# Performance work log

Hardware: AMD Instinct MI355X
Metric: run time of the kernel (lower is better)

The kernel has to match this reference:

```python
import jax, jax.numpy as jnp
import numpy as np

B, S, D, H = 2, 2048, 1024, 16
HD = D // H  # 64
EPS = 1e-8


def setup_inputs() -> dict:
    key = jax.random.key(0)
    ks = jax.random.split(key, 9)
    hidden_states = jax.random.normal(ks[0], (B, S, D), dtype=jnp.float32)
    # rotary tables: standard RoPE angles over half the head dim
    pos = jnp.arange(S, dtype=jnp.float32)[:, None]
    inv_freq = 1.0 / (10000.0 ** (jnp.arange(0, HD, 2, dtype=jnp.float32) / HD))  # [HD/2]
    ang = pos * inv_freq[None, :]  # [S, HD/2]
    sin = jnp.sin(ang)[None, None]  # [1,1,S,HD/2]
    cos = jnp.cos(ang)[None, None]
    s = 1.0 / np.sqrt(D)
    wq = jax.random.normal(ks[1], (D, D), dtype=jnp.float32) * s
    wk = jax.random.normal(ks[2], (D, D), dtype=jnp.float32) * s
    wv = jax.random.normal(ks[3], (D, D), dtype=jnp.float32) * s
    wo = jax.random.normal(ks[4], (D, D), dtype=jnp.float32) * s
    bo = jnp.zeros((D,), dtype=jnp.float32)
    scale = jnp.ones((D,), dtype=jnp.float32)
    return {"hidden_states": hidden_states, "sin": sin, "cos": cos,
            "wq": wq, "wk": wk, "wv": wv, "wo": wo, "bo": bo, "scale": scale}


def _heads(x):
    # [B,S,D] -> [B,H,S,HD]
    return x.reshape(B, S, H, HD).transpose(0, 2, 1, 3)


def _rotary(x, sin, cos):
    # interleaved RoPE: even/odd pairs
    x1, x2 = x[..., 0::2], x[..., 1::2]
    out = jnp.stack([x1 * cos - x2 * sin, x2 * cos + x1 * sin], axis=-1)
    return out.reshape(x.shape)


def reference(hidden_states, sin, cos, wq, wk, wv, wo, bo, scale):
    q = _rotary(_heads(hidden_states @ wq.T), sin, cos)
    k = _rotary(_heads(hidden_states @ wk.T), sin, cos)
    v = _rotary(_heads(hidden_states @ wv.T), sin, cos)
    scores = jnp.einsum("bhqd,bhkd->bhqk", q, k) / np.sqrt(HD)
    probs = jax.nn.softmax(scores, axis=-1)
    ctx = jnp.einsum("bhqk,bhkd->bhqd", probs, v)
    ctx = ctx.transpose(0, 2, 1, 3).reshape(B, S, D)
    out = ctx @ wo.T + bo
    x = out + hidden_states
    # RMSNorm: x / (||x||/sqrt(d) + eps) * scale
    rms = jnp.linalg.norm(x, axis=-1, keepdims=True) / np.sqrt(D)
    return scale * (x / (rms + EPS))
```

## Files before the change

### kernel.cpp

```cpp
#include <hip/hip_runtime.h>
#include <cmath>

#define BB 2
#define SS 2048
#define DD 1024
#define HH 16
#define HDIM 64
#define KDIM 1024
#define EPSF 1e-8f
#define QSCALE 0.18033688f

typedef __attribute__((ext_vector_type(8))) short bf16x8;
typedef __attribute__((ext_vector_type(4))) float f32x4;
typedef __attribute__((ext_vector_type(16))) float f32x16;

__device__ __forceinline__ ushort f2bf(float x) {
    unsigned u = __builtin_bit_cast(unsigned, x);
    u += 0x7FFFu + ((u >> 16) & 1u);
    return (ushort)(u >> 16);
}

__device__ __forceinline__ unsigned pack_bf16_trunc(float a, float b) {
    return __builtin_amdgcn_perm(__builtin_bit_cast(unsigned, b),
                                 __builtin_bit_cast(unsigned, a), 0x07060302u);
}

__device__ __forceinline__ float exp2_fast(float x) {
    float r;
    asm("v_exp_f32 %0, %1" : "=v"(r) : "v"(x));
    return r;
}

__device__ __forceinline__ void gload_lds16(const ushort* g, ushort* l) {
    __builtin_amdgcn_global_load_lds(
        (const __attribute__((address_space(1))) unsigned*)g,
        (__attribute__((address_space(3))) unsigned*)l, 16, 0, 0);
}

__global__ __launch_bounds__(256) void conv_all(
    const float* __restrict__ hs, const float* __restrict__ wq,
    const float* __restrict__ wk, const float* __restrict__ wv,
    const float* __restrict__ wo, ushort* __restrict__ dst)
{
    const int i = blockIdx.x * 256 + threadIdx.x;
    const int HS4 = (BB * SS * DD) / 4;
    const int W4 = (DD * DD) / 4;
    const float* src;
    int off;
    if (i < HS4) { src = hs; off = i; }
    else {
        const int j = i - HS4;
        const int seg = j / W4;
        off = j - seg * W4;
        src = (seg == 0) ? wq : (seg == 1) ? wk : (seg == 2) ? wv : wo;
    }
    const float4 v = ((const float4*)src)[off];
    ushort4 o;
    o.x = f2bf(v.x); o.y = f2bf(v.y); o.z = f2bf(v.z); o.w = f2bf(v.w);
    ((ushort4*)dst)[i] = o;
}

__global__ __launch_bounds__(256) void gemm_qkv_mfma(
    const ushort* __restrict__ A,
    const ushort* __restrict__ Wq, const ushort* __restrict__ Wk,
    const ushort* __restrict__ Wv,
    const float* __restrict__ sinp, const float* __restrict__ cosp,
    ushort* __restrict__ Qb, ushort* __restrict__ Kb, ushort* __restrict__ Vtb)
{
    const int cb = blockIdx.y;
    const int z = cb >> 3;
    const int col0 = (cb & 7) * 128;
    const ushort* W = (z == 0) ? Wq : (z == 1) ? Wk : Wv;
    ushort* O = (z == 0) ? Qb : (z == 1) ? Kb : Vtb;
    const int row0 = blockIdx.x * 128;
    const float qs = (z == 0) ? QSCALE : 1.0f;

    __shared__ __align__(16) ushort As[128 * 32];
    __shared__ __align__(16) ushort Bs[128 * 32];

    const int tid = threadIdx.x;
    const int w = tid >> 6, lane = tid & 63;
    const int quad = lane >> 4, l15 = lane & 15;
    const int m_off = (w >> 1) * 64, n_off = (w & 1) * 64;

    f32x4 acc[4][4] = {};

    for (int k0 = 0; k0 < KDIM; k0 += 32) {
#pragma unroll
        for (int it = 0; it < 2; ++it) {
            const int L = (it * 4 + w) * 64 + lane;
            const int r = L >> 2, c8 = (L & 3) * 8;
            gload_lds16(A + (size_t)(row0 + r) * KDIM + k0 + c8, &As[L * 8]);
            gload_lds16(W + (size_t)(col0 + r) * KDIM + k0 + c8, &Bs[L * 8]);
        }
        __syncthreads();
        bf16x8 af[4], bfr[4];
#pragma unroll
        for (int i = 0; i < 4; ++i) {
            af[i]  = *(const bf16x8*)&As[(m_off + i * 16 + l15) * 32 + quad * 8];
            bfr[i] = *(const bf16x8*)&Bs[(n_off + i * 16 + l15) * 32 + quad * 8];
        }
#pragma unroll
        for (int i = 0; i < 4; ++i)
#pragma unroll
            for (int j = 0; j < 4; ++j)
                acc[i][j] = __builtin_amdgcn_mfma_f32_16x16x32_bf16(
                    af[i], bfr[j], acc[i][j], 0, 0, 0);
        __syncthreads();
    }

    const int b = (row0 + m_off) / SS;
#pragma unroll
    for (int mi = 0; mi < 4; ++mi) {
        const int mrow = row0 + m_off + mi * 16 + quad * 4;
#pragma unroll
        for (int ni = 0; ni < 4; ++ni) {
            const int c = col0 + n_off + ni * 16 + l15;
            const int h = c >> 6, e = c & 63;
            const int bh = b * HH + h;
            float outv[4];
#pragma unroll
            for (int r = 0; r < 4; ++r) {
                const int s = (mrow + r) & (SS - 1);
                const float sv = sinp[s * (HDIM / 2) + (e >> 1)];
                const float cv = cosp[s * (HDIM / 2) + (e >> 1)];
                const float v = acc[mi][ni][r];
                const float vp = __shfl_xor(v, 1);
                outv[r] = ((l15 & 1) ? (v * cv + vp * sv) : (v * cv - vp * sv)) * qs;
            }
            if (z < 2) {
#pragma unroll
                for (int r = 0; r < 4; ++r) {
                    const int s = (mrow + r) & (SS - 1);
                    const ushort mine = f2bf(outv[r]);
                    const ushort part = (ushort)__shfl_xor((int)mine, 1);
                    if (!(l15 & 1))
                        *(unsigned*)(O + ((size_t)(bh * SS + s)) * HDIM + e) =
                            (unsigned)mine | ((unsigned)part << 16);
                }
            } else {
                ushort4 pk;
                pk.x = f2bf(outv[0]); pk.y = f2bf(outv[1]);
                pk.z = f2bf(outv[2]); pk.w = f2bf(outv[3]);
                const int s0 = mrow & (SS - 1);
                *(ushort4*)(O + ((size_t)(bh * HDIM + e)) * SS + s0) = pk;
            }
        }
    }
}

__global__ __launch_bounds__(256) void attn_mfma(
    const ushort* __restrict__ Qb, const ushort* __restrict__ Kb,
    const ushort* __restrict__ Vtb, ushort* __restrict__ ctx)
{
    const int wg  = blockIdx.x;
    const int lin = (wg & 7) * 128 + (wg >> 3);
    const int bh   = lin >> 5;
    const int qblk = lin & 31;
    const int b = bh / HH, h = bh % HH;
    const int q0 = qblk * 64;
    const int tid = threadIdx.x;
    const int w = tid >> 6;
    const int lane = tid & 63;
    const int l31 = lane & 31;
    const int g = lane >> 5;
    const int strip = w >> 1;
    const int phase = w & 1;

    __shared__ __align__(16) ushort kvb[2][2][2][64][32];

    const ushort* Qh = Qb  + (size_t)bh * SS * HDIM;
    const ushort* Kh = Kb  + (size_t)bh * SS * HDIM;
    const ushort* Vh = Vtb + (size_t)bh * HDIM * SS;

    const int qrow = q0 + strip * 32 + l31;
    bf16x8 qf[4];
#pragma unroll
    for (int ks = 0; ks < 4; ++ks)
        qf[ks] = *(const bf16x8*)(Qh + (size_t)qrow * HDIM + ks * 16 + g * 8);

    f32x16 cacc[2] = {};
    float ls0 = 0.f, ls1 = 0.f, ls2 = 0.f, ls3 = 0.f;

    const int lr = lane >> 2;
    const int c16 = lane & 3;
    const int lc = c16 * 8;
    const int swc = (c16 ^ ((lr >> 1) & 3)) * 8;
    const int srow = w * 16 + lr;
    const int rsw = (l31 >> 1) & 3;

    uint4 rk0, rk1, rv0, rv1;

#define LOAD_STAGE(K0)                                                        \
    do {                                                                      \
        const ushort* Kp = Kh + (size_t)((K0) + srow) * HDIM + lc;            \
        const ushort* Vp = Vh + (size_t)srow * SS + (K0) + lc;                \
        rk0 = *(const uint4*)(Kp);                                            \
        rk1 = *(const uint4*)(Kp + 32);                                       \
        rv0 = *(const uint4*)(Vp);                                            \
        rv1 = *(const uint4*)(Vp + 32);                                       \
    } while (0)

#define WRITE_STAGE(bufi)                                                     \
    do {                                                                      \
        *(uint4*)&kvb[bufi][0][0][srow][swc] = rk0;                           \
        *(uint4*)&kvb[bufi][0][1][srow][swc] = rk1;                           \
        *(uint4*)&kvb[bufi][1][0][srow][swc] = rv0;                           \
        *(uint4*)&kvb[bufi][1][1][srow][swc] = rv1;                           \
    } while (0)

    const int NT = SS / 64;

    LOAD_STAGE(0);
    WRITE_STAGE(0);
    LOAD_STAGE(64);

    for (int t = 0; t < NT; ++t) {
        __syncthreads();
        const int cur = t & 1;

        bf16x8 kf[4];
#pragma unroll
        for (int ks = 0; ks < 4; ++ks)
            kf[ks] = *(const bf16x8*)&kvb[cur][0][ks >> 1]
                [phase * 32 + l31][(((ks & 1) * 2 + g) ^ rsw) * 8];

        if (t + 1 < NT) WRITE_STAGE(cur ^ 1);
        if (t + 2 < NT) LOAD_STAGE((t + 2) * 64);

        f32x16 sacc = {};
        __builtin_amdgcn_s_setprio(1);
#pragma unroll
        for (int ks = 0; ks < 4; ++ks)
            sacc = __builtin_amdgcn_mfma_f32_32x32x16_bf16(
                kf[ks], qf[ks], sacc, 0, 0, 0);
        __builtin_amdgcn_s_setprio(0);

        unsigned pk[8];
#pragma unroll
        for (int i = 0; i < 8; ++i) {
            const float pa = exp2_fast(sacc[2 * i]);
            const float pb = exp2_fast(sacc[2 * i + 1]);
            if ((i & 3) == 0) ls0 += pa + pb;
            else if ((i & 3) == 1) ls1 += pa + pb;
            else if ((i & 3) == 2) ls2 += pa + pb;
            else ls3 += pa + pb;
            pk[i] = pack_bf16_trunc(pa, pb);
        }

#pragma unroll
        for (int ks = 0; ks < 2; ++ks) {
            const int bq = ks * 4;
            unsigned a0 = pk[bq + 0], a1 = pk[bq + 1];
            unsigned b0 = pk[bq + 2], b1 = pk[bq + 3];
            asm("v_permlane32_swap_b32 %0, %1" : "+v"(a0), "+v"(b0));
            asm("v_permlane32_swap_b32 %0, %1" : "+v"(a1), "+v"(b1));
            union { unsigned u[4]; bf16x8 v; } pf;
            pf.u[0] = a0; pf.u[1] = a1; pf.u[2] = b0; pf.u[3] = b1;
            __builtin_amdgcn_s_setprio(1);
#pragma unroll
            for (int dt = 0; dt < 2; ++dt) {
                const bf16x8 vf = *(const bf16x8*)&kvb[cur][1][phase]
                    [dt * 32 + l31][((ks * 2 + g) ^ rsw) * 8];
                cacc[dt] = __builtin_amdgcn_mfma_f32_32x32x16_bf16(
                    vf, pf.v, cacc[dt], 0, 0, 0);
            }
            __builtin_amdgcn_s_setprio(0);
        }
    }

    float lsum = (ls0 + ls1) + (ls2 + ls3);
    lsum += __shfl_xor(lsum, 32);

    __syncthreads();
    float* mlds = (float*)kvb;
    const int mbase = strip * 2112 + lane * 33;
    if (phase == 1) {
#pragma unroll
        for (int dt = 0; dt < 2; ++dt)
#pragma unroll
            for (int i = 0; i < 16; ++i) mlds[mbase + dt * 16 + i] = cacc[dt][i];
        mlds[mbase + 32] = lsum;
    }
    __syncthreads();
    if (phase == 0) {
#pragma unroll
        for (int dt = 0; dt < 2; ++dt)
#pragma unroll
            for (int i = 0; i < 16; ++i) cacc[dt][i] += mlds[mbase + dt * 16 + i];
        lsum += mlds[mbase + 32];
        const float inv = 1.f / lsum;

        const size_t obase = ((size_t)(b * SS + qrow)) * DD + h * HDIM;
#pragma unroll
        for (int dt = 0; dt < 2; ++dt)
#pragma unroll
            for (int t = 0; t < 4; ++t) {
                ushort4 o;
                o.x = f2bf(cacc[dt][t * 4 + 0] * inv);
                o.y = f2bf(cacc[dt][t * 4 + 1] * inv);
                o.z = f2bf(cacc[dt][t * 4 + 2] * inv);
                o.w = f2bf(cacc[dt][t * 4 + 3] * inv);
                *(ushort4*)(ctx + obase + dt * 32 + t * 8 + g * 4) = o;
            }
    }
#undef LOAD_STAGE
#undef WRITE_STAGE
}

__global__ __launch_bounds__(256) void gemm_out_mfma(
    const ushort* __restrict__ A, const ushort* __restrict__ W,
    const float* __restrict__ bias, float* __restrict__ Out)
{
    const int row0 = blockIdx.x * 128;
    const int col0 = blockIdx.y * 64;

    __shared__ __align__(16) ushort As[128 * 32];
    __shared__ __align__(16) ushort Bs[64 * 32];

    const int tid = threadIdx.x;
    const int w = tid >> 6, lane = tid & 63;
    const int quad = lane >> 4, l15 = lane & 15;
    const int m_off = (w >> 1) * 64, n_off = (w & 1) * 32;

    f32x4 acc[4][2] = {};

    for (int k0 = 0; k0 < KDIM; k0 += 32) {
#pragma unroll
        for (int it = 0; it < 2; ++it) {
            const int L = (it * 4 + w) * 64 + lane;
            const int r = L >> 2, c8 = (L & 3) * 8;
            gload_lds16(A + (size_t)(row0 + r) * KDIM + k0 + c8, &As[L * 8]);
        }
        {
            const int L = w * 64 + lane;
            const int r = L >> 2, c8 = (L & 3) * 8;
            gload_lds16(W + (size_t)(col0 + r) * KDIM + k0 + c8, &Bs[L * 8]);
        }
        __syncthreads();
        bf16x8 af[4], bfr[2];
#pragma unroll
        for (int i = 0; i < 4; ++i)
            af[i] = *(const bf16x8*)&As[(m_off + i * 16 + l15) * 32 + quad * 8];
#pragma unroll
        for (int j = 0; j < 2; ++j)
            bfr[j] = *(const bf16x8*)&Bs[(n_off + j * 16 + l15) * 32 + quad * 8];
#pragma unroll
        for (int i = 0; i < 4; ++i)
#pragma unroll
            for (int j = 0; j < 2; ++j)
                acc[i][j] = __builtin_amdgcn_mfma_f32_16x16x32_bf16(
                    af[i], bfr[j], acc[i][j], 0, 0, 0);
        __syncthreads();
    }

#pragma unroll
    for (int mi = 0; mi < 4; ++mi) {
        const int mrow = row0 + m_off + mi * 16 + quad * 4;
#pragma unroll
        for (int ni = 0; ni < 2; ++ni) {
            const int c = col0 + n_off + ni * 16 + l15;
            const float bv = bias[c];
#pragma unroll
            for (int r = 0; r < 4; ++r)
                Out[(size_t)(mrow + r) * DD + c] = acc[mi][ni][r] + bv;
        }
    }
}

__global__ __launch_bounds__(256) void resid_rmsnorm(
    const float* __restrict__ proj, const float* __restrict__ hs,
    const float* __restrict__ scale, float* __restrict__ out)
{
    const int t = blockIdx.x;
    const int tid = threadIdx.x;
    const size_t base = (size_t)t * DD + tid * 4;

    const float4 p4 = *(const float4*)(proj + base);
    const float4 h4 = *(const float4*)(hs + base);
    float x0 = p4.x + h4.x, x1 = p4.y + h4.y, x2 = p4.z + h4.z, x3 = p4.w + h4.w;
    float ss = x0 * x0 + x1 * x1 + x2 * x2 + x3 * x3;

#pragma unroll
    for (int off = 1; off < 64; off <<= 1) ss += __shfl_xor(ss, off);

    __shared__ float wsum[4];
    if ((tid & 63) == 0) wsum[tid >> 6] = ss;
    __syncthreads();
    const float total = wsum[0] + wsum[1] + wsum[2] + wsum[3];
    const float inv = 1.f / (sqrtf(total * (1.f / DD)) + EPSF);

    const float4 s4 = *(const float4*)(scale + tid * 4);
    float4 o;
    o.x = s4.x * x0 * inv;
    o.y = s4.y * x1 * inv;
    o.z = s4.z * x2 * inv;
    o.w = s4.w * x3 * inv;
    *(float4*)(out + base) = o;
}

extern "C" void kernel_launch(void* const* d_in, const int* in_sizes, int n_in,
                              void* d_out, int out_size, void* d_ws, size_t ws_size,
                              hipStream_t stream) {
    const float* hs    = (const float*)d_in[0];
    const float* sinp  = (const float*)d_in[1];
    const float* cosp  = (const float*)d_in[2];
    const float* wq    = (const float*)d_in[3];
    const float* wk    = (const float*)d_in[4];
    const float* wv    = (const float*)d_in[5];
    const float* wo    = (const float*)d_in[6];
    const float* bo    = (const float*)d_in[7];
    const float* scale = (const float*)d_in[8];
    float* out = (float*)d_out;

    unsigned char* wsb = (unsigned char*)d_ws;
    const size_t MAT = (size_t)BB * SS * DD;
    const size_t WN  = (size_t)DD * DD;
    ushort* Abf = (ushort*)wsb;
    ushort* Wqb = Abf + MAT;
    ushort* Wkb = Wqb + WN;
    ushort* Wvb = Wkb + WN;
    ushort* Wob = Wvb + WN;
    ushort* Qb  = Wob + WN;
    ushort* Kb  = Qb + MAT;
    ushort* Vtb = Kb + MAT;
    ushort* ctxb = Vtb + MAT;
    float* proj = (float*)(ctxb + MAT);

    const int nconv4 = (int)((MAT + 4 * WN) / 4);
    conv_all<<<dim3(nconv4 / 256), 256, 0, stream>>>(hs, wq, wk, wv, wo, Abf);

    gemm_qkv_mfma<<<dim3(32, 24), 256, 0, stream>>>(Abf, Wqb, Wkb, Wvb,
                                                    sinp, cosp, Qb, Kb, Vtb);
    attn_mfma<<<dim3(32 * BB * HH), 256, 0, stream>>>(Qb, Kb, Vtb, ctxb);
    gemm_out_mfma<<<dim3(32, 16), 256, 0, stream>>>(ctxb, Wob, bo, proj);
    resid_rmsnorm<<<dim3(BB * SS), 256, 0, stream>>>(proj, hs, scale, out);
}
```

Before: 208.1 us.

## Double attention query tile per workgroup to reuse K/V tiles across 128 queries

Each attention workgroup now handles 128 query rows instead of 64. Every wave computes two 32-row query strips against the same K/V fragments loaded from shared memory, which halves the global and LDS K/V traffic per query and gives the MFMA units more independent work. The grid shrinks to 512 workgroups and launch bounds request 2 blocks per SIMD. The cost is roughly doubled accumulator register pressure and fewer workgroups to spread over the CUs. The epilogue merges the two phase halves with an extra pair of barriers per strip.

```diff
diff --git a/kernel.cpp b/kernel.cpp
--- a/kernel.cpp
+++ b/kernel.cpp
@@ -149,16 +149,16 @@
     }
 }
 
-__global__ __launch_bounds__(256) void attn_mfma(
+__global__ __launch_bounds__(256, 2) void attn_mfma(
     const ushort* __restrict__ Qb, const ushort* __restrict__ Kb,
     const ushort* __restrict__ Vtb, ushort* __restrict__ ctx)
 {
     const int wg  = blockIdx.x;
-    const int lin = (wg & 7) * 128 + (wg >> 3);
-    const int bh   = lin >> 5;
-    const int qblk = lin & 31;
+    const int lin = (wg & 7) * 64 + (wg >> 3);
+    const int bh   = lin >> 4;
+    const int qblk = lin & 15;
     const int b = bh / HH, h = bh % HH;
-    const int q0 = qblk * 64;
+    const int q0 = qblk * 128;
     const int tid = threadIdx.x;
     const int w = tid >> 6;
     const int lane = tid & 63;
@@ -173,14 +173,17 @@
     const ushort* Kh = Kb  + (size_t)bh * SS * HDIM;
     const ushort* Vh = Vtb + (size_t)bh * HDIM * SS;
 
-    const int qrow = q0 + strip * 32 + l31;
-    bf16x8 qf[4];
-#pragma unroll
-    for (int ks = 0; ks < 4; ++ks)
-        qf[ks] = *(const bf16x8*)(Qh + (size_t)qrow * HDIM + ks * 16 + g * 8);
-
-    f32x16 cacc[2] = {};
-    float ls0 = 0.f, ls1 = 0.f, ls2 = 0.f, ls3 = 0.f;
+    const int qrowA = q0 + strip * 64 + l31;
+    const int qrowB = qrowA + 32;
+    bf16x8 qf[2][4];
+#pragma unroll
+    for (int ks = 0; ks < 4; ++ks) {
+        qf[0][ks] = *(const bf16x8*)(Qh + (size_t)qrowA * HDIM + ks * 16 + g * 8);
+        qf[1][ks] = *(const bf16x8*)(Qh + (size_t)qrowB * HDIM + ks * 16 + g * 8);
+    }
+
+    f32x16 cacc[2][2] = {};
+    float ls0a = 0.f, ls0b = 0.f, ls1a = 0.f, ls1b = 0.f;
 
     const int lr = lane >> 2;
     const int c16 = lane & 3;
@@ -228,81 +231,101 @@
         if (t + 1 < NT) WRITE_STAGE(cur ^ 1);
         if (t + 2 < NT) LOAD_STAGE((t + 2) * 64);
 
-        f32x16 sacc = {};
+        f32x16 sacc0 = {}, sacc1 = {};
         __builtin_amdgcn_s_setprio(1);
 #pragma unroll
-        for (int ks = 0; ks < 4; ++ks)
-            sacc = __builtin_amdgcn_mfma_f32_32x32x16_bf16(
-                kf[ks], qf[ks], sacc, 0, 0, 0);
+        for (int ks = 0; ks < 4; ++ks) {
+            sacc0 = __builtin_amdgcn_mfma_f32_32x32x16_bf16(
+                kf[ks], qf[0][ks], sacc0, 0, 0, 0);
+            sacc1 = __builtin_amdgcn_mfma_f32_32x32x16_bf16(
+                kf[ks], qf[1][ks], sacc1, 0, 0, 0);
+        }
         __builtin_amdgcn_s_setprio(0);
 
-        unsigned pk[8];
+        unsigned pk[2][8];
 #pragma unroll
         for (int i = 0; i < 8; ++i) {
-            const float pa = exp2_fast(sacc[2 * i]);
-            const float pb = exp2_fast(sacc[2 * i + 1]);
-            if ((i & 3) == 0) ls0 += pa + pb;
-            else if ((i & 3) == 1) ls1 += pa + pb;
-            else if ((i & 3) == 2) ls2 += pa + pb;
-            else ls3 += pa + pb;
-            pk[i] = pack_bf16_trunc(pa, pb);
+            const float pa0 = exp2_fast(sacc0[2 * i]);
+            const float pb0 = exp2_fast(sacc0[2 * i + 1]);
+            const float pa1 = exp2_fast(sacc1[2 * i]);
+            const float pb1 = exp2_fast(sacc1[2 * i + 1]);
+            if (i & 1) { ls0b += pa0 + pb0; ls1b += pa1 + pb1; }
+            else       { ls0a += pa0 + pb0; ls1a += pa1 + pb1; }
+            pk[0][i] = pack_bf16_trunc(pa0, pb0);
+            pk[1][i] = pack_bf16_trunc(pa1, pb1);
         }
 
 #pragma unroll
         for (int ks = 0; ks < 2; ++ks) {
             const int bq = ks * 4;
-            unsigned a0 = pk[bq + 0], a1 = pk[bq + 1];
-            unsigned b0 = pk[bq + 2], b1 = pk[bq + 3];
-            asm("v_permlane32_swap_b32 %0, %1" : "+v"(a0), "+v"(b0));
-            asm("v_permlane32_swap_b32 %0, %1" : "+v"(a1), "+v"(b1));
-            union { unsigned u[4]; bf16x8 v; } pf;
-            pf.u[0] = a0; pf.u[1] = a1; pf.u[2] = b0; pf.u[3] = b1;
+            unsigned a00 = pk[0][bq + 0], a01 = pk[0][bq + 1];
+            unsigned b00 = pk[0][bq + 2], b01 = pk[0][bq + 3];
+            unsigned a10 = pk[1][bq + 0], a11 = pk[1][bq + 1];
+            unsigned b10 = pk[1][bq + 2], b11 = pk[1][bq + 3];
+            asm("v_permlane32_swap_b32 %0, %1" : "+v"(a00), "+v"(b00));
+            asm("v_permlane32_swap_b32 %0, %1" : "+v"(a01), "+v"(b01));
+            asm("v_permlane32_swap_b32 %0, %1" : "+v"(a10), "+v"(b10));
+            asm("v_permlane32_swap_b32 %0, %1" : "+v"(a11), "+v"(b11));
+            union { unsigned u[4]; bf16x8 v; } pf0, pf1;
+            pf0.u[0] = a00; pf0.u[1] = a01; pf0.u[2] = b00; pf0.u[3] = b01;
+            pf1.u[0] = a10; pf1.u[1] = a11; pf1.u[2] = b10; pf1.u[3] = b11;
             __builtin_amdgcn_s_setprio(1);
 #pragma unroll
             for (int dt = 0; dt < 2; ++dt) {
                 const bf16x8 vf = *(const bf16x8*)&kvb[cur][1][phase]
                     [dt * 32 + l31][((ks * 2 + g) ^ rsw) * 8];
-                cacc[dt] = __builtin_amdgcn_mfma_f32_32x32x16_bf16(
-                    vf, pf.v, cacc[dt], 0, 0, 0);
+                cacc[0][dt] = __builtin_amdgcn_mfma_f32_32x32x16_bf16(
+                    vf, pf0.v, cacc[0][dt], 0, 0, 0);
+                cacc[1][dt] = __builtin_amdgcn_mfma_f32_32x32x16_bf16(
+                    vf, pf1.v, cacc[1][dt], 0, 0, 0);
             }
             __builtin_amdgcn_s_setprio(0);
         }
     }
 
-    float lsum = (ls0 + ls1) + (ls2 + ls3);
-    lsum += __shfl_xor(lsum, 32);
-
-    __syncthreads();
+    float lsq[2];
+    lsq[0] = ls0a + ls0b;
+    lsq[1] = ls1a + ls1b;
+    lsq[0] += __shfl_xor(lsq[0], 32);
+    lsq[1] += __shfl_xor(lsq[1], 32);
+
     float* mlds = (float*)kvb;
     const int mbase = strip * 2112 + lane * 33;
-    if (phase == 1) {
-#pragma unroll
-        for (int dt = 0; dt < 2; ++dt)
-#pragma unroll
-            for (int i = 0; i < 16; ++i) mlds[mbase + dt * 16 + i] = cacc[dt][i];
-        mlds[mbase + 32] = lsum;
-    }
-    __syncthreads();
-    if (phase == 0) {
-#pragma unroll
-        for (int dt = 0; dt < 2; ++dt)
-#pragma unroll
-            for (int i = 0; i < 16; ++i) cacc[dt][i] += mlds[mbase + dt * 16 + i];
-        lsum += mlds[mbase + 32];
-        const float inv = 1.f / lsum;
-
-        const size_t obase = ((size_t)(b * SS + qrow)) * DD + h * HDIM;
-#pragma unroll
-        for (int dt = 0; dt < 2; ++dt)
-#pragma unroll
-            for (int t = 0; t < 4; ++t) {
-                ushort4 o;
-                o.x = f2bf(cacc[dt][t * 4 + 0] * inv);
-                o.y = f2bf(cacc[dt][t * 4 + 1] * inv);
-                o.z = f2bf(cacc[dt][t * 4 + 2] * inv);
-                o.w = f2bf(cacc[dt][t * 4 + 3] * inv);
-                *(ushort4*)(ctx + obase + dt * 32 + t * 8 + g * 4) = o;
-            }
+#pragma unroll
+    for (int qs = 0; qs < 2; ++qs) {
+        __syncthreads();
+        if (phase == 1) {
+#pragma unroll
+            for (int dt = 0; dt < 2; ++dt)
+#pragma unroll
+                for (int i = 0; i < 16; ++i)
+                    mlds[mbase + dt * 16 + i] = cacc[qs][dt][i];
+            mlds[mbase + 32] = lsq[qs];
+        }
+        __syncthreads();
+        if (phase == 0) {
+            f32x16 cf[2];
+#pragma unroll
+            for (int dt = 0; dt < 2; ++dt)
+#pragma unroll
+                for (int i = 0; i < 16; ++i)
+                    cf[dt][i] = cacc[qs][dt][i] + mlds[mbase + dt * 16 + i];
+            const float inv = 1.f / (lsq[qs] + mlds[mbase + 32]);
+
+            const int qrow = (qs == 0) ? qrowA : qrowB;
+            const size_t obase = ((size_t)(b * SS + qrow)) * DD + h * HDIM;
+#pragma unroll
+            for (int dt = 0; dt < 2; ++dt)
+#pragma unroll
+                for (int tt = 0; tt < 4; ++tt) {
+                    ushort4 o;
+                    o.x = f2bf(cf[dt][tt * 4 + 0] * inv);
+                    o.y = f2bf(cf[dt][tt * 4 + 1] * inv);
+                    o.z = f2bf(cf[dt][tt * 4 + 2] * inv);
+                    o.w = f2bf(cf[dt][tt * 4 + 3] * inv);
+                    *(ushort4*)(ctx + obase + dt * 32 + tt * 8 + g * 4) = o;
+                }
+        }
     }
 #undef LOAD_STAGE
 #undef WRITE_STAGE
@@ -432,7 +455,7 @@
 
     gemm_qkv_mfma<<<dim3(32, 24), 256, 0, stream>>>(Abf, Wqb, Wkb, Wvb,
                                                     sinp, cosp, Qb, Kb, Vtb);
-    attn_mfma<<<dim3(32 * BB * HH), 256, 0, stream>>>(Qb, Kb, Vtb, ctxb);
+    attn_mfma<<<dim3(512), 256, 0, stream>>>(Qb, Kb, Vtb, ctxb);
     gemm_out_mfma<<<dim3(32, 16), 256, 0, stream>>>(ctxb, Wob, bo, proj);
     resid_rmsnorm<<<dim3(BB * SS), 256, 0, stream>>>(proj, hs, scale, out);
 }
```

Result: faster. 195.3 us (-6.2%).
